# Kernel optimization log

Measured on AMD Instinct MI355X. Metric: run time of the kernel, lower is better.

Reference implementation:

```python
import jax, jax.numpy as jnp
import numpy as np

EPS_NORM = 1e-12   # F.normalize eps (denominator clamp)
EPS_PD = 1e-6      # F.pairwise_distance eps (added to the difference)
MARGIN = 0.3

B, D = 8192, 512


def setup_inputs() -> dict:
    key = jax.random.key(0)
    x = jax.random.normal(key, (B, D * 2), dtype=jnp.float32).reshape(B, 2, D)
    return {"x": x}


def reference(x):
    # x: [B, 2, D]  (anchor, positive)
    a = x[:, 0, :]
    p = x[:, 1, :]
    a = a / jnp.maximum(jnp.linalg.norm(a, axis=1, keepdims=True), EPS_NORM)
    p = p / jnp.maximum(jnp.linalg.norm(p, axis=1, keepdims=True), EPS_NORM)
    b, d = a.shape

    # output[i, j] = -||a_i - p_j + EPS_PD||^2, expanded so the BxB matrix
    # comes from one GEMM instead of a [B, D, B] broadcasted difference.
    sa2 = jnp.sum(a * a, axis=1)               # [B]
    sp2 = jnp.sum(p * p, axis=1)               # [B]
    dot = a @ p.T                              # [B, B]
    sa = jnp.sum(a, axis=1)                    # [B]
    sp = jnp.sum(p, axis=1)                    # [B]
    d2 = (sa2[:, None] + sp2[None, :] - 2.0 * dot
          + 2.0 * EPS_PD * (sa[:, None] - sp[None, :]) + d * (EPS_PD * EPS_PD))
    sim = -d2                                  # [B, B] similarity (detached in torch)

    # mineHardNegative with hard_rank=0, hard_prob=1: top-1 of descending sort
    # after removing the self index -> argmax over the row with diag masked.
    sim = jnp.where(jnp.eye(b, dtype=bool), -jnp.inf, sim)
    negidx = jnp.argmax(sim, axis=1)           # [B] int
    n = p[negidx]                              # hard negatives, [B, D]

    pos_d = jnp.linalg.norm(a - p + EPS_PD, axis=1)
    neg_d = jnp.linalg.norm(a - n + EPS_PD, axis=1)
    nloss = jnp.mean(jax.nn.relu(pos_d ** 2 - neg_d ** 2 + MARGIN))
    return nloss
```

## Files before the change

kernel.cpp:

```cpp
#include <hip/hip_runtime.h>
#include <stdint.h>
#include <math.h>

#define Bn 8192
#define Dn 512
#define EPSN 1e-12f
#define EPSP 1e-6f
#define MARG 0.3f
#define QS 256.0f
#define ISQ (2.0f / 65536.0f)


#define TKB 64
#define NKT (Dn / TKB)

typedef int   int4v __attribute__((ext_vector_type(4)));
typedef float f32x4 __attribute__((ext_vector_type(4)));

__device__ __forceinline__ void async16(const void* g, void* l) {
    __builtin_amdgcn_global_load_lds(
        (const __attribute__((address_space(1))) void*)g,
        (__attribute__((address_space(3))) void*)l,
        16, 0, 0);
}

__device__ __forceinline__ unsigned key32(float s) {
    union { float f; unsigned u; } c; c.f = s;
    return (c.u & 0x80000000u) ? ~c.u : (c.u | 0x80000000u);
}
__device__ __forceinline__ float unkey32(unsigned k) {
    union { unsigned u; float f; } c;
    c.u = (k & 0x80000000u) ? (k ^ 0x80000000u) : ~k;
    return c.f;
}

__global__ __launch_bounds__(256) void k_normalize(
    const float* __restrict__ x,
    uint8_t* __restrict__ a_i8, uint8_t* __restrict__ p_i8,
    float* __restrict__ cterm, float* __restrict__ rowconst,
    unsigned* __restrict__ rowmax)
{
    const int wave = threadIdx.x >> 6;
    const int lane = threadIdx.x & 63;
    const int i = blockIdx.x * 4 + wave;

    const float* srcA = x + (size_t)i * (2 * Dn) + lane * 8;
    const float* srcP = srcA + Dn;
    float4 a0 = ((const float4*)srcA)[0];
    float4 a1 = ((const float4*)srcA)[1];
    float4 p0 = ((const float4*)srcP)[0];
    float4 p1 = ((const float4*)srcP)[1];
    float va[8] = {a0.x, a0.y, a0.z, a0.w, a1.x, a1.y, a1.z, a1.w};
    float vp[8] = {p0.x, p0.y, p0.z, p0.w, p1.x, p1.y, p1.z, p1.w};

    float ssa = 0.f, ssp = 0.f;
#pragma unroll
    for (int j = 0; j < 8; ++j) { ssa += va[j] * va[j]; ssp += vp[j] * vp[j]; }
#pragma unroll
    for (int m = 1; m < 64; m <<= 1) {
        ssa += __shfl_xor(ssa, m);
        ssp += __shfl_xor(ssp, m);
    }
    const float sa = 1.0f / fmaxf(sqrtf(ssa), EPSN);
    const float sp = 1.0f / fmaxf(sqrtf(ssp), EPSN);

    float oa[8], op[8];
    float s1p = 0.f, s2p = 0.f, s1a = 0.f, s2a = 0.f, pos = 0.f;
#pragma unroll
    for (int j = 0; j < 8; ++j) {
        oa[j] = va[j] * sa;
        op[j] = vp[j] * sp;
        s1p += op[j]; s2p += op[j] * op[j];
        s1a += oa[j]; s2a += oa[j] * oa[j];
        const float u = oa[j] - op[j] + EPSP;
        pos += u * u;
    }

    uint64_t pka = 0, pkp = 0;
#pragma unroll
    for (int j = 0; j < 8; ++j) {
        int qa = (int)rintf(oa[j] * QS);
        int qp = (int)rintf(op[j] * QS);
        qa = qa > 127 ? 127 : (qa < -127 ? -127 : qa);
        qp = qp > 127 ? 127 : (qp < -127 ? -127 : qp);
        pka |= (uint64_t)(uint8_t)qa << (8 * j);
        pkp |= (uint64_t)(uint8_t)qp << (8 * j);
    }
    *(uint64_t*)(a_i8 + (size_t)i * Dn + lane * 8) = pka;
    *(uint64_t*)(p_i8 + (size_t)i * Dn + lane * 8) = pkp;

#pragma unroll
    for (int m = 1; m < 64; m <<= 1) {
        s1p += __shfl_xor(s1p, m);
        s2p += __shfl_xor(s2p, m);
        s1a += __shfl_xor(s1a, m);
        s2a += __shfl_xor(s2a, m);
        pos += __shfl_xor(pos, m);
    }
    if (lane == 0) {
        cterm[i] = -s2p + 2.0f * EPSP * s1p;
        rowconst[i] = pos - s2a - 2.0f * EPSP * s1a
                      - (float)Dn * EPSP * EPSP + MARG;
        rowmax[i] = 0u;
    }
}

__global__ __launch_bounds__(512, 2) void k_gemm_argmax(
    const uint8_t* __restrict__ a_i8, const uint8_t* __restrict__ p_i8,
    const float* __restrict__ cterm,
    unsigned* __restrict__ rowmax)
{
    __shared__ __align__(16) uint8_t As[4][256 * TKB];
    __shared__ __align__(16) uint8_t Bs[4][256 * TKB];
    __shared__ unsigned smx[2][256];

    const int t = threadIdx.x;
    const int wave = t >> 6;
    const int lane = t & 63;
    const int q = lane >> 4;
    const int m16 = lane & 15;
    const int wr = wave >> 2;
    const int wc = wave & 3;
    const int j0 = blockIdx.y * 256;
    const int i0 = blockIdx.x * 256;

    const int rr = t >> 2;
    const int gg = ((t & 3) ^ ((t >> 3) & 3)) * 16;
    const uint8_t* gA0 = p_i8 + (size_t)(j0 + rr) * Dn + gg;
    const uint8_t* gA1 = p_i8 + (size_t)(j0 + 128 + rr) * Dn + gg;
    const uint8_t* gB0 = a_i8 + (size_t)(i0 + rr) * Dn + gg;
    const uint8_t* gB1 = a_i8 + (size_t)(i0 + 128 + rr) * Dn + gg;
    const int ldsOff = wave * 1024;

    const int sl = (q ^ ((m16 >> 1) & 3)) * 16;
    const int aOff = (wr * 128 + m16) * TKB + sl;
    const int bOff = (wc * 64 + m16) * TKB + sl;

    auto stage1 = [&](int slot, int kb, int h) {
        switch (h) {
        case 0: async16(gA0 + kb, &As[slot][ldsOff]);        break;
        case 1: async16(gA1 + kb, &As[slot][8192 + ldsOff]); break;
        case 2: async16(gB0 + kb, &Bs[slot][ldsOff]);        break;
        case 3: async16(gB1 + kb, &Bs[slot][8192 + ldsOff]); break;
        }
    };

    int4v acc[8][4];
#pragma unroll
    for (int a = 0; a < 8; ++a)
#pragma unroll
        for (int b = 0; b < 4; ++b) acc[a][b] = (int4v){0, 0, 0, 0};

#pragma unroll
    for (int h = 0; h < 4; ++h) stage1(0, 0, h);
#pragma unroll
    for (int h = 0; h < 4; ++h) stage1(1, TKB, h);
    asm volatile("s_waitcnt vmcnt(4)" ::: "memory");
    __builtin_amdgcn_s_barrier();

#pragma unroll
    for (int kt = 0; kt < NKT; ++kt) {
        const int slot = kt & 3;
        const uint8_t* pa = &As[slot][aOff];
        const uint8_t* pb = &Bs[slot][bOff];

        int4v af[8], bf[4];
        bf[0] = *(const int4v*)(pb + 0 * 1024);
        bf[1] = *(const int4v*)(pb + 1 * 1024);
        bf[2] = *(const int4v*)(pb + 2 * 1024);
        bf[3] = *(const int4v*)(pb + 3 * 1024);
        af[0] = *(const int4v*)(pa + 0 * 1024);
        af[1] = *(const int4v*)(pa + 1 * 1024);
        __builtin_amdgcn_sched_barrier(0);
        af[2] = *(const int4v*)(pa + 2 * 1024);
        af[3] = *(const int4v*)(pa + 3 * 1024);
        __builtin_amdgcn_sched_barrier(0);
        af[4] = *(const int4v*)(pa + 4 * 1024);
        af[5] = *(const int4v*)(pa + 5 * 1024);
        __builtin_amdgcn_sched_barrier(0);
        af[6] = *(const int4v*)(pa + 6 * 1024);
        af[7] = *(const int4v*)(pa + 7 * 1024);
        __builtin_amdgcn_sched_barrier(0);

        asm volatile("s_waitcnt lgkmcnt(6)" ::: "memory");
        __builtin_amdgcn_sched_barrier(0);
        __builtin_amdgcn_s_setprio(1);
#pragma unroll
        for (int nt = 0; nt < 4; ++nt)
            acc[0][nt] = __builtin_amdgcn_mfma_i32_16x16x64_i8(
                af[0], bf[nt], acc[0][nt], 0, 0, 0);
#pragma unroll
        for (int nt = 0; nt < 4; ++nt)
            acc[1][nt] = __builtin_amdgcn_mfma_i32_16x16x64_i8(
                af[1], bf[nt], acc[1][nt], 0, 0, 0);

        asm volatile("s_waitcnt lgkmcnt(4)" ::: "memory");
        __builtin_amdgcn_sched_barrier(0);
#pragma unroll
        for (int nt = 0; nt < 4; ++nt)
            acc[2][nt] = __builtin_amdgcn_mfma_i32_16x16x64_i8(
                af[2], bf[nt], acc[2][nt], 0, 0, 0);
#pragma unroll
        for (int nt = 0; nt < 4; ++nt)
            acc[3][nt] = __builtin_amdgcn_mfma_i32_16x16x64_i8(
                af[3], bf[nt], acc[3][nt], 0, 0, 0);

        asm volatile("s_waitcnt lgkmcnt(2)" ::: "memory");
        __builtin_amdgcn_sched_barrier(0);
#pragma unroll
        for (int nt = 0; nt < 4; ++nt)
            acc[4][nt] = __builtin_amdgcn_mfma_i32_16x16x64_i8(
                af[4], bf[nt], acc[4][nt], 0, 0, 0);
#pragma unroll
        for (int nt = 0; nt < 4; ++nt)
            acc[5][nt] = __builtin_amdgcn_mfma_i32_16x16x64_i8(
                af[5], bf[nt], acc[5][nt], 0, 0, 0);

        asm volatile("s_waitcnt lgkmcnt(0)" ::: "memory");
        __builtin_amdgcn_sched_barrier(0);
        if (kt + 2 < NKT) {
#pragma unroll
            for (int h = 0; h < 4; ++h) stage1((kt + 2) & 3, (kt + 2) * TKB, h);
        }
#pragma unroll
        for (int nt = 0; nt < 4; ++nt)
            acc[6][nt] = __builtin_amdgcn_mfma_i32_16x16x64_i8(
                af[6], bf[nt], acc[6][nt], 0, 0, 0);
#pragma unroll
        for (int nt = 0; nt < 4; ++nt)
            acc[7][nt] = __builtin_amdgcn_mfma_i32_16x16x64_i8(
                af[7], bf[nt], acc[7][nt], 0, 0, 0);
        __builtin_amdgcn_s_setprio(0);

        if (kt + 2 < NKT)
            asm volatile("s_waitcnt vmcnt(4)" ::: "memory");
        else if (kt + 2 == NKT)
            asm volatile("s_waitcnt vmcnt(0)" ::: "memory");
        if (kt + 1 < NKT) __builtin_amdgcn_s_barrier();
    }

    f32x4 cj[8];
#pragma unroll
    for (int mt = 0; mt < 8; ++mt)
        cj[mt] = *(const f32x4*)(cterm + j0 + wr * 128 + mt * 16 + q * 4);

    unsigned kv[4];
    const bool diag = (i0 == j0);
    if (!diag) {
#pragma unroll
        for (int nt = 0; nt < 4; ++nt) {
            float mx = -3.4e38f;
#pragma unroll
            for (int mt = 0; mt < 8; ++mt)
#pragma unroll
                for (int v = 0; v < 4; ++v)
                    mx = fmaxf(mx, ISQ * (float)acc[mt][nt][v] + cj[mt][v]);
            kv[nt] = key32(mx);
        }
    } else {
#pragma unroll
        for (int nt = 0; nt < 4; ++nt) {
            const int dtarget = wc * 64 + nt * 16 + m16 - wr * 128 - q * 4;
            float mx = -3.4e38f;
#pragma unroll
            for (int mt = 0; mt < 8; ++mt)
#pragma unroll
                for (int v = 0; v < 4; ++v) {
                    const float sc = ISQ * (float)acc[mt][nt][v] + cj[mt][v];
                    mx = (mt * 16 + v == dtarget) ? mx : fmaxf(mx, sc);
                }
            kv[nt] = key32(mx);
        }
    }

#pragma unroll
    for (int nt = 0; nt < 4; ++nt) {
#pragma unroll
        for (int msk = 16; msk < 64; msk <<= 1) {
            const unsigned o = (unsigned)__shfl_xor((int)kv[nt], msk);
            kv[nt] = o > kv[nt] ? o : kv[nt];
        }
    }
    if (lane < 16) {
#pragma unroll
        for (int nt = 0; nt < 4; ++nt)
            smx[wr][wc * 64 + nt * 16 + m16] = kv[nt];
    }
    __syncthreads();
    if (t < 256) {
        const unsigned k0 = smx[0][t];
        const unsigned k1 = smx[1][t];
        atomicMax(&rowmax[i0 + t], k0 > k1 ? k0 : k1);
    }
}

__global__ __launch_bounds__(1024) void k_final(
    const unsigned* __restrict__ rowmax,
    const float* __restrict__ rowconst,
    float* __restrict__ out)
{
    __shared__ float smf[16];
    float s = 0.f;
    for (int k = threadIdx.x; k < Bn; k += 1024)
        s += fmaxf(rowconst[k] + unkey32(rowmax[k]), 0.f);
#pragma unroll
    for (int msk = 1; msk < 64; msk <<= 1) s += __shfl_xor(s, msk);
    if ((threadIdx.x & 63) == 0) smf[threadIdx.x >> 6] = s;
    __syncthreads();
    if (threadIdx.x == 0) {
        float tot = 0.f;
#pragma unroll
        for (int w = 0; w < 16; ++w) tot += smf[w];
        out[0] = tot * (1.0f / Bn);
    }
}

extern "C" void kernel_launch(void* const* d_in, const int* in_sizes, int n_in,
                              void* d_out, int out_size, void* d_ws, size_t ws_size,
                              hipStream_t stream)
{
    const float* x = (const float*)d_in[0];
    char* ws = (char*)d_ws;
    uint8_t*  a_i8     = (uint8_t*)(ws + 0);
    uint8_t*  p_i8     = (uint8_t*)(ws + 4194304);
    float*    cterm    = (float*)(ws + 8388608);
    float*    rowconst = (float*)(ws + 8421376);
    unsigned* rowmax   = (unsigned*)(ws + 8454144);
    float*    out      = (float*)d_out;

    k_normalize<<<2048, 256, 0, stream>>>(x, a_i8, p_i8, cterm, rowconst, rowmax);
    k_gemm_argmax<<<dim3(Bn / 256, Bn / 256), 512, 0, stream>>>(
        a_i8, p_i8, cterm, rowmax);
    k_final<<<1, 1024, 0, stream>>>(rowmax, rowconst, out);
}
```

Before: 113.6 us.

## Load GEMM B operand directly into double-buffered registers, bypassing LDS

The i8 anchor tile (B operand) is no longer staged through shared memory. Each wave now loads its 64-row slice straight from global memory into registers, double-buffered one k-step ahead, while only the positive tile keeps the async LDS pipeline. This halves shared-memory use and removes the LDS reads for B fragments. In exchange, the two waves sharing a column group fetch the same global data twice, and the extra buffers raise register pressure under the 512x2 launch bound.

```diff
diff --git a/kernel.cpp b/kernel.cpp
--- a/kernel.cpp
+++ b/kernel.cpp
@@ -111,7 +111,6 @@
     unsigned* __restrict__ rowmax)
 {
     __shared__ __align__(16) uint8_t As[4][256 * TKB];
-    __shared__ __align__(16) uint8_t Bs[4][256 * TKB];
     __shared__ unsigned smx[2][256];
 
     const int t = threadIdx.x;
@@ -128,21 +127,16 @@
     const int gg = ((t & 3) ^ ((t >> 3) & 3)) * 16;
     const uint8_t* gA0 = p_i8 + (size_t)(j0 + rr) * Dn + gg;
     const uint8_t* gA1 = p_i8 + (size_t)(j0 + 128 + rr) * Dn + gg;
-    const uint8_t* gB0 = a_i8 + (size_t)(i0 + rr) * Dn + gg;
-    const uint8_t* gB1 = a_i8 + (size_t)(i0 + 128 + rr) * Dn + gg;
     const int ldsOff = wave * 1024;
 
     const int sl = (q ^ ((m16 >> 1) & 3)) * 16;
     const int aOff = (wr * 128 + m16) * TKB + sl;
-    const int bOff = (wc * 64 + m16) * TKB + sl;
-
-    auto stage1 = [&](int slot, int kb, int h) {
-        switch (h) {
-        case 0: async16(gA0 + kb, &As[slot][ldsOff]);        break;
-        case 1: async16(gA1 + kb, &As[slot][8192 + ldsOff]); break;
-        case 2: async16(gB0 + kb, &Bs[slot][ldsOff]);        break;
-        case 3: async16(gB1 + kb, &Bs[slot][8192 + ldsOff]); break;
-        }
+
+    const uint8_t* gBreg = a_i8 + (size_t)(i0 + wc * 64 + m16) * Dn + q * 16;
+
+    auto stageA = [&](int slot, int kb) {
+        async16(gA0 + kb, &As[slot][ldsOff]);
+        async16(gA1 + kb, &As[slot][8192 + ldsOff]);
     };
 
     int4v acc[8][4];
@@ -151,24 +145,35 @@
 #pragma unroll
         for (int b = 0; b < 4; ++b) acc[a][b] = (int4v){0, 0, 0, 0};
 
-#pragma unroll
-    for (int h = 0; h < 4; ++h) stage1(0, 0, h);
-#pragma unroll
-    for (int h = 0; h < 4; ++h) stage1(1, TKB, h);
-    asm volatile("s_waitcnt vmcnt(4)" ::: "memory");
+    int4v bfA[4], bfB[4];
+
+    stageA(0, 0);
+#pragma unroll
+    for (int nt = 0; nt < 4; ++nt)
+        bfA[nt] = *(const int4v*)(gBreg + nt * 16 * Dn);
+    __builtin_amdgcn_sched_barrier(0);
+    stageA(1, TKB);
+    __builtin_amdgcn_sched_barrier(0);
+    asm volatile("s_waitcnt vmcnt(2)" ::: "memory");
     __builtin_amdgcn_s_barrier();
 
 #pragma unroll
     for (int kt = 0; kt < NKT; ++kt) {
         const int slot = kt & 3;
         const uint8_t* pa = &As[slot][aOff];
-        const uint8_t* pb = &Bs[slot][bOff];
-
-        int4v af[8], bf[4];
-        bf[0] = *(const int4v*)(pb + 0 * 1024);
-        bf[1] = *(const int4v*)(pb + 1 * 1024);
-        bf[2] = *(const int4v*)(pb + 2 * 1024);
-        bf[3] = *(const int4v*)(pb + 3 * 1024);
+        int4v* bfc = (kt & 1) ? bfB : bfA;
+        int4v* bfn = (kt & 1) ? bfA : bfB;
+
+        if (kt + 1 < NKT) {
+#pragma unroll
+            for (int nt = 0; nt < 4; ++nt)
+                bfn[nt] = *(const int4v*)(gBreg + nt * 16 * Dn + (kt + 1) * TKB);
+        }
+        __builtin_amdgcn_sched_barrier(0);
+        if (kt + 2 < NKT) stageA((kt + 2) & 3, (kt + 2) * TKB);
+        __builtin_amdgcn_sched_barrier(0);
+
+        int4v af[8];
         af[0] = *(const int4v*)(pa + 0 * 1024);
         af[1] = *(const int4v*)(pa + 1 * 1024);
         __builtin_amdgcn_sched_barrier(0);
@@ -188,52 +193,48 @@
 #pragma unroll
         for (int nt = 0; nt < 4; ++nt)
             acc[0][nt] = __builtin_amdgcn_mfma_i32_16x16x64_i8(
-                af[0], bf[nt], acc[0][nt], 0, 0, 0);
+                af[0], bfc[nt], acc[0][nt], 0, 0, 0);
 #pragma unroll
         for (int nt = 0; nt < 4; ++nt)
             acc[1][nt] = __builtin_amdgcn_mfma_i32_16x16x64_i8(
-                af[1], bf[nt], acc[1][nt], 0, 0, 0);
+                af[1], bfc[nt], acc[1][nt], 0, 0, 0);
 
         asm volatile("s_waitcnt lgkmcnt(4)" ::: "memory");
         __builtin_amdgcn_sched_barrier(0);
 #pragma unroll
         for (int nt = 0; nt < 4; ++nt)
             acc[2][nt] = __builtin_amdgcn_mfma_i32_16x16x64_i8(
-                af[2], bf[nt], acc[2][nt], 0, 0, 0);
+                af[2], bfc[nt], acc[2][nt], 0, 0, 0);
 #pragma unroll
         for (int nt = 0; nt < 4; ++nt)
             acc[3][nt] = __builtin_amdgcn_mfma_i32_16x16x64_i8(
-                af[3], bf[nt], acc[3][nt], 0, 0, 0);
+                af[3], bfc[nt], acc[3][nt], 0, 0, 0);
 
         asm volatile("s_waitcnt lgkmcnt(2)" ::: "memory");
         __builtin_amdgcn_sched_barrier(0);
 #pragma unroll
         for (int nt = 0; nt < 4; ++nt)
             acc[4][nt] = __builtin_amdgcn_mfma_i32_16x16x64_i8(
-                af[4], bf[nt], acc[4][nt], 0, 0, 0);
+                af[4], bfc[nt], acc[4][nt], 0, 0, 0);
 #pragma unroll
         for (int nt = 0; nt < 4; ++nt)
             acc[5][nt] = __builtin_amdgcn_mfma_i32_16x16x64_i8(
-                af[5], bf[nt], acc[5][nt], 0, 0, 0);
+                af[5], bfc[nt], acc[5][nt], 0, 0, 0);
 
         asm volatile("s_waitcnt lgkmcnt(0)" ::: "memory");
         __builtin_amdgcn_sched_barrier(0);
-        if (kt + 2 < NKT) {
-#pragma unroll
-            for (int h = 0; h < 4; ++h) stage1((kt + 2) & 3, (kt + 2) * TKB, h);
-        }
 #pragma unroll
         for (int nt = 0; nt < 4; ++nt)
             acc[6][nt] = __builtin_amdgcn_mfma_i32_16x16x64_i8(
-                af[6], bf[nt], acc[6][nt], 0, 0, 0);
+                af[6], bfc[nt], acc[6][nt], 0, 0, 0);
 #pragma unroll
         for (int nt = 0; nt < 4; ++nt)
             acc[7][nt] = __builtin_amdgcn_mfma_i32_16x16x64_i8(
-                af[7], bf[nt], acc[7][nt], 0, 0, 0);
+                af[7], bfc[nt], acc[7][nt], 0, 0, 0);
         __builtin_amdgcn_s_setprio(0);
 
         if (kt + 2 < NKT)
-            asm volatile("s_waitcnt vmcnt(4)" ::: "memory");
+            asm volatile("s_waitcnt vmcnt(2)" ::: "memory");
         else if (kt + 2 == NKT)
             asm volatile("s_waitcnt vmcnt(0)" ::: "memory");
         if (kt + 1 < NKT) __builtin_amdgcn_s_barrier();
```

Measured after the change: 129.8 us. +14.3%, slower.

## Halve GEMM tile height, use a two-stage buffer and target four blocks per CU

Applied to the files above, without the earlier changes.

Shrinks the int8 GEMM+argmax tile from 256x256 to 128(j)x256(i) and cuts the LDS ring from four stages to two. The kernel now prefetches one stage ahead with a full vmcnt(0) wait and a barrier each k-step, and launch bounds go from 2 to 4 blocks per CU. The goal is higher occupancy and half the accumulator registers, so several blocks can hide latency instead of the deep per-block prefetch. The cost is more global/L2 traffic for the reloaded A operand, a shallower pipeline with stricter waits, and twice as many blocks writing the row-max atomics. The diagonal masking logic is adjusted for the new offset between i and j tiles.

```diff
diff --git a/kernel.cpp b/kernel.cpp
--- a/kernel.cpp
+++ b/kernel.cpp
@@ -105,13 +105,13 @@
     }
 }
 
-__global__ __launch_bounds__(512, 2) void k_gemm_argmax(
+__global__ __launch_bounds__(512, 4) void k_gemm_argmax(
     const uint8_t* __restrict__ a_i8, const uint8_t* __restrict__ p_i8,
     const float* __restrict__ cterm,
     unsigned* __restrict__ rowmax)
 {
-    __shared__ __align__(16) uint8_t As[4][256 * TKB];
-    __shared__ __align__(16) uint8_t Bs[4][256 * TKB];
+    __shared__ __align__(16) uint8_t As[2][128 * TKB];
+    __shared__ __align__(16) uint8_t Bs[2][256 * TKB];
     __shared__ unsigned smx[2][256];
 
     const int t = threadIdx.x;
@@ -121,137 +121,105 @@
     const int m16 = lane & 15;
     const int wr = wave >> 2;
     const int wc = wave & 3;
-    const int j0 = blockIdx.y * 256;
+    const int j0 = blockIdx.y * 128;
     const int i0 = blockIdx.x * 256;
 
     const int rr = t >> 2;
     const int gg = ((t & 3) ^ ((t >> 3) & 3)) * 16;
     const uint8_t* gA0 = p_i8 + (size_t)(j0 + rr) * Dn + gg;
-    const uint8_t* gA1 = p_i8 + (size_t)(j0 + 128 + rr) * Dn + gg;
     const uint8_t* gB0 = a_i8 + (size_t)(i0 + rr) * Dn + gg;
     const uint8_t* gB1 = a_i8 + (size_t)(i0 + 128 + rr) * Dn + gg;
     const int ldsOff = wave * 1024;
 
     const int sl = (q ^ ((m16 >> 1) & 3)) * 16;
-    const int aOff = (wr * 128 + m16) * TKB + sl;
+    const int aOff = (wr * 64 + m16) * TKB + sl;
     const int bOff = (wc * 64 + m16) * TKB + sl;
 
-    auto stage1 = [&](int slot, int kb, int h) {
-        switch (h) {
-        case 0: async16(gA0 + kb, &As[slot][ldsOff]);        break;
-        case 1: async16(gA1 + kb, &As[slot][8192 + ldsOff]); break;
-        case 2: async16(gB0 + kb, &Bs[slot][ldsOff]);        break;
-        case 3: async16(gB1 + kb, &Bs[slot][8192 + ldsOff]); break;
-        }
+    auto stage = [&](int slot, int kb) {
+        async16(gA0 + kb, &As[slot][ldsOff]);
+        async16(gB0 + kb, &Bs[slot][ldsOff]);
+        async16(gB1 + kb, &Bs[slot][8192 + ldsOff]);
     };
 
-    int4v acc[8][4];
-#pragma unroll
-    for (int a = 0; a < 8; ++a)
+    int4v acc[4][4];
+#pragma unroll
+    for (int a = 0; a < 4; ++a)
 #pragma unroll
         for (int b = 0; b < 4; ++b) acc[a][b] = (int4v){0, 0, 0, 0};
 
-#pragma unroll
-    for (int h = 0; h < 4; ++h) stage1(0, 0, h);
-#pragma unroll
-    for (int h = 0; h < 4; ++h) stage1(1, TKB, h);
-    asm volatile("s_waitcnt vmcnt(4)" ::: "memory");
+    stage(0, 0);
+    asm volatile("s_waitcnt vmcnt(0)" ::: "memory");
     __builtin_amdgcn_s_barrier();
 
 #pragma unroll
     for (int kt = 0; kt < NKT; ++kt) {
-        const int slot = kt & 3;
-        const uint8_t* pa = &As[slot][aOff];
-        const uint8_t* pb = &Bs[slot][bOff];
-
-        int4v af[8], bf[4];
+        const int cur = kt & 1;
+        if (kt + 1 < NKT) stage(cur ^ 1, (kt + 1) * TKB);
+        __builtin_amdgcn_sched_barrier(0);
+
+        const uint8_t* pa = &As[cur][aOff];
+        const uint8_t* pb = &Bs[cur][bOff];
+        int4v af[4], bf[4];
         bf[0] = *(const int4v*)(pb + 0 * 1024);
         bf[1] = *(const int4v*)(pb + 1 * 1024);
         bf[2] = *(const int4v*)(pb + 2 * 1024);
         bf[3] = *(const int4v*)(pb + 3 * 1024);
         af[0] = *(const int4v*)(pa + 0 * 1024);
+        __builtin_amdgcn_sched_barrier(0);
         af[1] = *(const int4v*)(pa + 1 * 1024);
         __builtin_amdgcn_sched_barrier(0);
         af[2] = *(const int4v*)(pa + 2 * 1024);
+        __builtin_amdgcn_sched_barrier(0);
         af[3] = *(const int4v*)(pa + 3 * 1024);
         __builtin_amdgcn_sched_barrier(0);
-        af[4] = *(const int4v*)(pa + 4 * 1024);
-        af[5] = *(const int4v*)(pa + 5 * 1024);
-        __builtin_amdgcn_sched_barrier(0);
-        af[6] = *(const int4v*)(pa + 6 * 1024);
-        af[7] = *(const int4v*)(pa + 7 * 1024);
-        __builtin_amdgcn_sched_barrier(0);
-
-        asm volatile("s_waitcnt lgkmcnt(6)" ::: "memory");
+
+        asm volatile("s_waitcnt lgkmcnt(3)" ::: "memory");
         __builtin_amdgcn_sched_barrier(0);
         __builtin_amdgcn_s_setprio(1);
 #pragma unroll
         for (int nt = 0; nt < 4; ++nt)
             acc[0][nt] = __builtin_amdgcn_mfma_i32_16x16x64_i8(
                 af[0], bf[nt], acc[0][nt], 0, 0, 0);
+        asm volatile("s_waitcnt lgkmcnt(2)" ::: "memory");
+        __builtin_amdgcn_sched_barrier(0);
 #pragma unroll
         for (int nt = 0; nt < 4; ++nt)
             acc[1][nt] = __builtin_amdgcn_mfma_i32_16x16x64_i8(
                 af[1], bf[nt], acc[1][nt], 0, 0, 0);
-
-        asm volatile("s_waitcnt lgkmcnt(4)" ::: "memory");
+        asm volatile("s_waitcnt lgkmcnt(1)" ::: "memory");
         __builtin_amdgcn_sched_barrier(0);
 #pragma unroll
         for (int nt = 0; nt < 4; ++nt)
             acc[2][nt] = __builtin_amdgcn_mfma_i32_16x16x64_i8(
                 af[2], bf[nt], acc[2][nt], 0, 0, 0);
+        asm volatile("s_waitcnt lgkmcnt(0)" ::: "memory");
+        __builtin_amdgcn_sched_barrier(0);
 #pragma unroll
         for (int nt = 0; nt < 4; ++nt)
             acc[3][nt] = __builtin_amdgcn_mfma_i32_16x16x64_i8(
                 af[3], bf[nt], acc[3][nt], 0, 0, 0);
-
-        asm volatile("s_waitcnt lgkmcnt(2)" ::: "memory");
-        __builtin_amdgcn_sched_barrier(0);
-#pragma unroll
-        for (int nt = 0; nt < 4; ++nt)
-            acc[4][nt] = __builtin_amdgcn_mfma_i32_16x16x64_i8(
-                af[4], bf[nt], acc[4][nt], 0, 0, 0);
-#pragma unroll
-        for (int nt = 0; nt < 4; ++nt)
-            acc[5][nt] = __builtin_amdgcn_mfma_i32_16x16x64_i8(
-                af[5], bf[nt], acc[5][nt], 0, 0, 0);
-
-        asm volatile("s_waitcnt lgkmcnt(0)" ::: "memory");
-        __builtin_amdgcn_sched_barrier(0);
-        if (kt + 2 < NKT) {
-#pragma unroll
-            for (int h = 0; h < 4; ++h) stage1((kt + 2) & 3, (kt + 2) * TKB, h);
+        __builtin_amdgcn_s_setprio(0);
+
+        if (kt + 1 < NKT) {
+            asm volatile("s_waitcnt vmcnt(0)" ::: "memory");
+            __builtin_amdgcn_s_barrier();
         }
-#pragma unroll
-        for (int nt = 0; nt < 4; ++nt)
-            acc[6][nt] = __builtin_amdgcn_mfma_i32_16x16x64_i8(
-                af[6], bf[nt], acc[6][nt], 0, 0, 0);
-#pragma unroll
-        for (int nt = 0; nt < 4; ++nt)
-            acc[7][nt] = __builtin_amdgcn_mfma_i32_16x16x64_i8(
-                af[7], bf[nt], acc[7][nt], 0, 0, 0);
-        __builtin_amdgcn_s_setprio(0);
-
-        if (kt + 2 < NKT)
-            asm volatile("s_waitcnt vmcnt(4)" ::: "memory");
-        else if (kt + 2 == NKT)
-            asm volatile("s_waitcnt vmcnt(0)" ::: "memory");
-        if (kt + 1 < NKT) __builtin_amdgcn_s_barrier();
-    }
-
-    f32x4 cj[8];
-#pragma unroll
-    for (int mt = 0; mt < 8; ++mt)
-        cj[mt] = *(const f32x4*)(cterm + j0 + wr * 128 + mt * 16 + q * 4);
+    }
+
+    f32x4 cj[4];
+#pragma unroll
+    for (int mt = 0; mt < 4; ++mt)
+        cj[mt] = *(const f32x4*)(cterm + j0 + wr * 64 + mt * 16 + q * 4);
 
     unsigned kv[4];
-    const bool diag = (i0 == j0);
+    const int dj = i0 - j0;
+    const bool diag = (dj == 0) || (dj == -128);
     if (!diag) {
 #pragma unroll
         for (int nt = 0; nt < 4; ++nt) {
             float mx = -3.4e38f;
 #pragma unroll
-            for (int mt = 0; mt < 8; ++mt)
+            for (int mt = 0; mt < 4; ++mt)
 #pragma unroll
                 for (int v = 0; v < 4; ++v)
                     mx = fmaxf(mx, ISQ * (float)acc[mt][nt][v] + cj[mt][v]);
@@ -260,10 +228,10 @@
     } else {
 #pragma unroll
         for (int nt = 0; nt < 4; ++nt) {
-            const int dtarget = wc * 64 + nt * 16 + m16 - wr * 128 - q * 4;
+            const int dtarget = dj + wc * 64 + nt * 16 + m16 - wr * 64 - q * 4;
             float mx = -3.4e38f;
 #pragma unroll
-            for (int mt = 0; mt < 8; ++mt)
+            for (int mt = 0; mt < 4; ++mt)
 #pragma unroll
                 for (int v = 0; v < 4; ++v) {
                     const float sc = ISQ * (float)acc[mt][nt][v] + cj[mt][v];
@@ -329,7 +297,7 @@
     float*    out      = (float*)d_out;
 
     k_normalize<<<2048, 256, 0, stream>>>(x, a_i8, p_i8, cterm, rowconst, rowmax);
-    k_gemm_argmax<<<dim3(Bn / 256, Bn / 256), 512, 0, stream>>>(
+    k_gemm_argmax<<<dim3(Bn / 256, Bn / 128), 512, 0, stream>>>(
         a_i8, p_i8, cterm, rowmax);
     k_final<<<1, 1024, 0, stream>>>(rowmax, rowconst, out);
 }
```

After: 114.7 us. Within noise of the previous version (+1.0%).
